# Optimization experiments

Measured on AMD Instinct MI355X. Metric: run time of the kernel, lower is better.

The kernel has to match this reference:

```python
import jax, jax.numpy as jnp
import numpy as np

C_IN, C_OUT, G = 64, 64, 32
D_MODEL = C_IN + 4 * G            # 192
DI = 2 * D_MODEL                  # d_inner = 384 (expand=2)
N_STATE = 16
DT_RANK = (D_MODEL + 15) // 16    # 12
K_DIR = 4
B, H, W = 2, 64, 64


def setup_inputs() -> dict:
    key = jax.random.key(0)
    ks = jax.random.split(key, 16)
    rn = lambda k, shp, s=0.02: jax.random.normal(k, shp, jnp.float32) * s
    inp = {"x": jax.random.normal(ks[0], (B, C_IN, H, W), jnp.float32)}
    chans = [C_IN, C_IN + G, C_IN + 2 * G, C_IN + 3 * G]
    for i, ci in enumerate(chans):
        inp[f"c{i+1}_w"] = rn(ks[1 + i], (G, ci, 3, 3))
        inp[f"c{i+1}_b"] = jnp.zeros((G,), jnp.float32)
    inp["c5_w"] = rn(ks[5], (C_OUT, D_MODEL, 3, 3))
    inp["c5_b"] = jnp.zeros((C_OUT,), jnp.float32)
    inp["ln1_g"] = jnp.ones((D_MODEL,), jnp.float32)
    inp["ln1_b"] = jnp.zeros((D_MODEL,), jnp.float32)
    inp["in_proj_w"] = rn(ks[6], (2 * DI, D_MODEL))
    inp["dw_w"] = rn(ks[7], (DI, 1, 3, 3))          # depthwise conv kernel
    inp["dw_b"] = jnp.zeros((DI,), jnp.float32)
    inp["x_proj_w"] = rn(ks[8], (K_DIR, DT_RANK + 2 * N_STATE, DI))
    inp["dt_w"] = rn(ks[9], (K_DIR, DI, DT_RANK), 0.1)
    inp["dt_b"] = jax.random.uniform(ks[10], (K_DIR, DI), jnp.float32, -4.0, -2.0)
    inp["A_logs"] = jnp.log(jnp.tile(jnp.arange(1, N_STATE + 1, dtype=jnp.float32), (K_DIR, DI, 1)))
    inp["Ds"] = jnp.ones((K_DIR, DI), jnp.float32)
    inp["out_norm_g"] = jnp.ones((DI,), jnp.float32)
    inp["out_norm_b"] = jnp.zeros((DI,), jnp.float32)
    inp["out_proj_w"] = rn(ks[11], (D_MODEL, DI))
    return inp


def conv2d(x, w, b, groups=1):
    y = jax.lax.conv_general_dilated(x, w, (1, 1), 'SAME',
                                     feature_group_count=groups,
                                     dimension_numbers=('NCHW', 'OIHW', 'NCHW'))
    return y + b[None, :, None, None]


def layer_norm(x, g, b, eps=1e-5):
    mu = jnp.mean(x, -1, keepdims=True)
    var = jnp.var(x, -1, keepdims=True)
    return (x - mu) * jax.lax.rsqrt(var + eps) * g + b


def selective_scan(u, delta, A, Bm, Cm, D):
    # u, delta: (B,K,Dm,L); Bm, Cm: (B,K,N,L); A: (K,Dm,N); D: (K,Dm)
    uL = jnp.moveaxis(u, -1, 0)
    dL = jnp.moveaxis(delta, -1, 0)
    BL = jnp.moveaxis(Bm, -1, 0)
    CL = jnp.moveaxis(Cm, -1, 0)
    h0 = jnp.zeros(u.shape[:3] + (A.shape[-1],), u.dtype)  # (B,K,Dm,N)

    def step(h, inp):
        u_l, d_l, B_l, C_l = inp
        dA = jnp.exp(d_l[..., None] * A)                              # (B,K,Dm,N)
        h = dA * h + (d_l * u_l)[..., None] * B_l[:, :, None, :]
        y = jnp.einsum('bkdn,bkn->bkd', h, C_l)
        return h, y

    _, ys = jax.lax.scan(step, h0, (uL, dL, BL, CL))
    y = jnp.moveaxis(ys, 0, -1)                                       # (B,K,Dm,L)
    return y + D[None, :, :, None] * u


def vss_block(x, ln1_g, ln1_b, in_proj_w, dw_w, dw_b, x_proj_w, dt_w, dt_b,
              A_logs, Ds, out_norm_g, out_norm_b, out_proj_w):
    Bn, C, Hh, Ww = x.shape
    L = Hh * Ww
    di = in_proj_w.shape[0] // 2
    nst = A_logs.shape[-1]
    dtr = dt_w.shape[-1]
    xi = jnp.transpose(x, (0, 2, 3, 1))                               # BHWC
    xn = layer_norm(xi, ln1_g, ln1_b)
    xz = xn @ in_proj_w.T                                             # (B,H,W,2*di)
    xp, z = jnp.split(xz, 2, -1)
    xc = jnp.transpose(xp, (0, 3, 1, 2))                              # (B,di,H,W)
    xc = jax.nn.silu(conv2d(xc, dw_w, dw_b, groups=di))
    xf = xc.reshape(Bn, di, L)
    xt = jnp.transpose(xc, (0, 1, 3, 2)).reshape(Bn, di, L)
    xs = jnp.stack([xf, xt, xf[..., ::-1], xt[..., ::-1]], 1)         # (B,4,di,L)
    x_dbl = jnp.einsum('bkdl,kcd->bkcl', xs, x_proj_w)
    dts = jnp.einsum('bkrl,kdr->bkdl', x_dbl[:, :, :dtr], dt_w)
    Bs = x_dbl[:, :, dtr:dtr + nst]
    Cs = x_dbl[:, :, dtr + nst:]
    delta = jax.nn.softplus(dts + dt_b[None, :, :, None])
    A = -jnp.exp(A_logs)
    oy = selective_scan(xs, delta, A, Bs, Cs, Ds)                     # (B,4,di,L)
    inv = oy[:, 2:4, :, ::-1]
    wh = jnp.transpose(oy[:, 1].reshape(Bn, di, Ww, Hh), (0, 1, 3, 2)).reshape(Bn, di, L)
    iwh = jnp.transpose(inv[:, 1].reshape(Bn, di, Ww, Hh), (0, 1, 3, 2)).reshape(Bn, di, L)
    y = oy[:, 0] + inv[:, 0] + wh + iwh
    y = jnp.transpose(y, (0, 2, 1)).reshape(Bn, Hh, Ww, di)
    y = layer_norm(y, out_norm_g, out_norm_b)
    y = y * jax.nn.silu(z)
    out = xi + y @ out_proj_w.T                                       # residual (VSSBlock)
    return jnp.transpose(out, (0, 3, 1, 2))


def reference(x, c1_w, c1_b, c2_w, c2_b, c3_w, c3_b, c4_w, c4_b, c5_w, c5_b,
              ln1_g, ln1_b, in_proj_w, dw_w, dw_b, x_proj_w, dt_w, dt_b,
              A_logs, Ds, out_norm_g, out_norm_b, out_proj_w):
    lrelu = lambda t: jax.nn.leaky_relu(t, 0.01)
    x1 = lrelu(conv2d(x, c1_w, c1_b))
    x2 = lrelu(conv2d(jnp.concatenate([x, x1], 1), c2_w, c2_b))
    x3 = lrelu(conv2d(jnp.concatenate([x, x1, x2], 1), c3_w, c3_b))
    x4 = lrelu(conv2d(jnp.concatenate([x, x1, x2, x3], 1), c4_w, c4_b))
    f = jnp.concatenate([x, x1, x2, x3, x4], 1)                       # (B,192,H,W)
    sa = vss_block(f, ln1_g, ln1_b, in_proj_w, dw_w, dw_b, x_proj_w, dt_w, dt_b,
                   A_logs, Ds, out_norm_g, out_norm_b, out_proj_w)
    return conv2d(sa, c5_w, c5_b)
```

## Files before the change

### kernel.cpp

```cpp
#include <hip/hip_runtime.h>
#include <hip/hip_bf16.h>
#include <math.h>

static constexpr int LEN = 4096;
static constexpr int HN  = 64;
static constexpr int WN  = 64;
static constexpr int NB  = 2;
static constexpr int DM  = 192;
static constexpr int DIM = 384;
static constexpr int NST = 16;
static constexpr int DTR = 12;
static constexpr int KD  = 4;
static constexpr int NC  = 64;
static constexpr int CHL = LEN / NC;

typedef __attribute__((ext_vector_type(8))) short bfrag;
typedef __attribute__((ext_vector_type(4))) float facc;

__device__ __forceinline__ unsigned short f2bf(float x) {
    unsigned int u = __float_as_uint(x);
    return (unsigned short)((u + 0x7FFFu + ((u >> 16) & 1u)) >> 16);
}

__device__ __forceinline__ int maprow(int k, int gl) {
    int g = (k & 2) ? (LEN - 1 - gl) : gl;
    return (k & 1) ? (((g & 63) << 6) | (g >> 6)) : g;
}

__global__ void k_wtr(const float* __restrict__ w, float* __restrict__ wt,
                      int cin, int cout, int n)
{
    int idx = blockIdx.x * 256 + threadIdx.x;
    if (idx >= n) return;
    int ci = idx % cin; int r = idx / cin;
    int co = r % cout; int t = r / cout;
    wt[idx] = w[((size_t)(co * cin + ci)) * 9 + t];
}

__global__ void k_wxp(const float* __restrict__ xpw, float* __restrict__ WX)
{
    int idx = blockIdx.x * 256 + threadIdx.x;
    if (idx >= 192 * DIM) return;
    int row = idx / DIM, d = idx - row * DIM;
    int k = row / 48, c = row - k * 48;
    WX[idx] = (c < 44) ? xpw[((size_t)(k * 44 + c)) * DIM + d] : 0.f;
}

__global__ void k_tr_in(const float* __restrict__ x, float* __restrict__ FN)
{
    __shared__ float t[64][65];
    int b = blockIdx.y, r = blockIdx.x;
    int tid = threadIdx.x;
#pragma unroll
    for (int i = 0; i < 16; ++i) {
        int idx = (i << 8) + tid;
        int c = idx >> 6, xc = idx & 63;
        t[c][xc] = x[((size_t)(b * 64 + c)) * LEN + r * WN + xc];
    }
    __syncthreads();
#pragma unroll
    for (int i = 0; i < 16; ++i) {
        int idx = (i << 8) + tid;
        int px = idx >> 6, c = idx & 63;
        FN[((size_t)(b * LEN + r * WN + px)) * DM + c] = t[c][px];
    }
}

__global__ void __launch_bounds__(256) k_convmf(
    const float* __restrict__ in, int cbuf, int cin, int cout,
    const float* __restrict__ wt2,
    float* __restrict__ part)
{
    __shared__ unsigned short Asb[66][40];
    __shared__ unsigned short Bsb[3][32][40];
    int zz = blockIdx.z;
    int b = zz / 3, s = zz % 3;
    int y0 = blockIdx.x;
    int n0 = blockIdx.y << 5;
    int tid = threadIdx.x;
    int wv = tid >> 6, lane = tid & 63;
    int mb  = (wv & 1) << 5;
    int nbw = (wv >> 1) << 4;
    int lr = lane & 15, lq = lane >> 4;
    int y = y0 + s - 1;
    bool yok = (unsigned)y < (unsigned)HN;
    const float* inb = in + ((size_t)b * LEN + (size_t)y * WN) * cbuf;

    facc acc0 = (facc){0,0,0,0}, acc1 = (facc){0,0,0,0};

    for (int ci0 = 0; ci0 < cin; ci0 += 32) {
#pragma unroll
        for (int it = 0; it < 3; ++it) {
            int fi = (it << 8) + tid;
            if (fi < 528) {
                int px = fi >> 3, c4 = (fi & 7) << 2;
                int xx = px - 1;
                float4 v = make_float4(0.f, 0.f, 0.f, 0.f);
                if (yok && (unsigned)xx < (unsigned)WN)
                    v = *(const float4*)(inb + (size_t)xx * cbuf + ci0 + c4);
                ushort4 u; u.x = f2bf(v.x); u.y = f2bf(v.y); u.z = f2bf(v.z); u.w = f2bf(v.w);
                *(ushort4*)(&Asb[px][c4]) = u;
            }
        }
#pragma unroll
        for (int it = 0; it < 3; ++it) {
            int fi = (it << 8) + tid;
            int dx = fi >> 8; int rem = fi & 255;
            int oc = rem >> 3, c4 = (rem & 7) << 2;
            int t = s * 3 + dx;
            float4 v = *(const float4*)(wt2 + ((size_t)(t * cout + n0 + oc)) * cin + ci0 + c4);
            ushort4 u; u.x = f2bf(v.x); u.y = f2bf(v.y); u.z = f2bf(v.z); u.w = f2bf(v.w);
            *(ushort4*)(&Bsb[dx][oc][c4]) = u;
        }
        __syncthreads();
#pragma unroll
        for (int dx = 0; dx < 3; ++dx) {
            bfrag a0 = *(const bfrag*)(&Asb[mb + lr + dx][lq * 8]);
            bfrag a1 = *(const bfrag*)(&Asb[mb + 16 + lr + dx][lq * 8]);
            bfrag b0 = *(const bfrag*)(&Bsb[dx][nbw + lr][lq * 8]);
            acc0 = __builtin_amdgcn_mfma_f32_16x16x32_bf16(a0, b0, acc0, 0, 0, 0);
            acc1 = __builtin_amdgcn_mfma_f32_16x16x32_bf16(a1, b0, acc1, 0, 0, 0);
        }
        __syncthreads();
    }
    float* pb = part + (((size_t)(s * NB + b) * LEN) + y0 * WN) * cout + n0 + nbw + lr;
#pragma unroll
    for (int r = 0; r < 4; ++r) {
        int px0 = mb + lq * 4 + r;
        pb[(size_t)px0 * cout] = acc0[r];
        pb[(size_t)(px0 + 16) * cout] = acc1[r];
    }
}

__global__ void k_ep_nhwc(const float* __restrict__ part, const float* __restrict__ bias,
                          float* __restrict__ FN, int co0, float slope)
{
    int idx = blockIdx.x * 256 + threadIdx.x;
    int co = idx & 31, px = idx >> 5;
    const size_t S = (size_t)NB * LEN * 32;
    float v = part[idx] + part[S + idx] + part[2 * S + idx] + bias[co];
    v = v > 0.f ? v : v * slope;
    FN[(size_t)px * DM + co0 + co] = v;
}

__global__ void k_ep_pl_tr(const float* __restrict__ part, const float* __restrict__ bias,
                           float* __restrict__ out)
{
    __shared__ float t[64][65];
    int b = blockIdx.y, l0 = blockIdx.x << 6;
    int tid = threadIdx.x;
    const size_t S = (size_t)NB * LEN * 64;
#pragma unroll
    for (int i = 0; i < 16; ++i) {
        int idx = (i << 8) + tid;
        int px = idx >> 6, oc = idx & 63;
        size_t o = ((size_t)b * LEN + l0 + px) * 64 + oc;
        t[px][oc] = part[o] + part[S + o] + part[2 * S + o] + bias[oc];
    }
    __syncthreads();
#pragma unroll
    for (int i = 0; i < 16; ++i) {
        int idx = (i << 8) + tid;
        int oc = idx >> 6, px = idx & 63;
        out[((size_t)(b * 64 + oc)) * LEN + l0 + px] = t[px][oc];
    }
}

__global__ void k_ln(const float* __restrict__ FN, const float* __restrict__ g,
                     const float* __restrict__ be, float* __restrict__ xn)
{
    int lane = threadIdx.x & 63;
    int pix  = (blockIdx.x << 2) + (threadIdx.x >> 6);
    const float* fp = FN + (size_t)pix * DM;
    float v0 = fp[lane];
    float v1 = fp[lane + 64];
    float v2 = fp[lane + 128];
    float s = v0 + v1 + v2, ss = v0 * v0 + v1 * v1 + v2 * v2;
#pragma unroll
    for (int off = 1; off < 64; off <<= 1) { s += __shfl_xor(s, off); ss += __shfl_xor(ss, off); }
    float mu = s * (1.f / 192.f);
    float var = ss * (1.f / 192.f) - mu * mu;
    float rstd = rsqrtf(var + 1e-5f);
    float* op = xn + (size_t)pix * DM;
    op[lane]       = (v0 - mu) * rstd * g[lane]       + be[lane];
    op[lane + 64]  = (v1 - mu) * rstd * g[lane + 64]  + be[lane + 64];
    op[lane + 128] = (v2 - mu) * rstd * g[lane + 128] + be[lane + 128];
}

struct MfTile { facc a00, a01, a10, a11; int mb, nb, lr, lq; };

__device__ __forceinline__ MfTile mf_gemm_core(
    const float* __restrict__ A, int K, const float* __restrict__ Wt,
    int b, int l0, int n0, unsigned short (*Asb)[72], unsigned short (*Bsb)[72])
{
    int tid = threadIdx.x;
    MfTile t;
    t.a00 = (facc){0,0,0,0}; t.a01 = (facc){0,0,0,0};
    t.a10 = (facc){0,0,0,0}; t.a11 = (facc){0,0,0,0};
    int wv = tid >> 6, lane = tid & 63;
    t.mb = (wv & 1) << 5; t.nb = (wv >> 1) << 5;
    t.lr = lane & 15; t.lq = lane >> 4;

    for (int k0 = 0; k0 < K; k0 += 64) {
#pragma unroll
        for (int s = 0; s < 4; ++s) {
            int idx = (s << 8) + tid;
            int row = idx >> 4, c4 = (idx & 15) << 2;
            float4 av = *(const float4*)(A + ((size_t)b * LEN + l0 + row) * K + k0 + c4);
            ushort4 ua; ua.x = f2bf(av.x); ua.y = f2bf(av.y); ua.z = f2bf(av.z); ua.w = f2bf(av.w);
            *(ushort4*)(&Asb[row][c4]) = ua;
            float4 wvv = *(const float4*)(Wt + (size_t)(n0 + row) * K + k0 + c4);
            ushort4 ub; ub.x = f2bf(wvv.x); ub.y = f2bf(wvv.y); ub.z = f2bf(wvv.z); ub.w = f2bf(wvv.w);
            *(ushort4*)(&Bsb[row][c4]) = ub;
        }
        __syncthreads();
#pragma unroll
        for (int kk = 0; kk < 64; kk += 32) {
            bfrag a0 = *(const bfrag*)(&Asb[t.mb + t.lr][kk + t.lq * 8]);
            bfrag a1 = *(const bfrag*)(&Asb[t.mb + 16 + t.lr][kk + t.lq * 8]);
            bfrag b0 = *(const bfrag*)(&Bsb[t.nb + t.lr][kk + t.lq * 8]);
            bfrag b1 = *(const bfrag*)(&Bsb[t.nb + 16 + t.lr][kk + t.lq * 8]);
            t.a00 = __builtin_amdgcn_mfma_f32_16x16x32_bf16(a0, b0, t.a00, 0, 0, 0);
            t.a01 = __builtin_amdgcn_mfma_f32_16x16x32_bf16(a0, b1, t.a01, 0, 0, 0);
            t.a10 = __builtin_amdgcn_mfma_f32_16x16x32_bf16(a1, b0, t.a10, 0, 0, 0);
            t.a11 = __builtin_amdgcn_mfma_f32_16x16x32_bf16(a1, b1, t.a11, 0, 0, 0);
        }
        __syncthreads();
    }
    return t;
}

__device__ __forceinline__ void mf_store(
    facc v, float* __restrict__ Cp, const float* __restrict__ res,
    int b, int l0, int n0, int outC, int lr, int lq)
{
#pragma unroll
    for (int r = 0; r < 4; ++r) {
        int m = lq * 4 + r, n = lr;
        size_t o = ((size_t)b * LEN + l0 + m) * outC + n0 + n;
        float x = v[r];
        if (res) x += res[o];
        Cp[o] = x;
    }
}

__global__ void __launch_bounds__(256) k_gemm_mf(
    const float* __restrict__ A, int K, const float* __restrict__ Wt,
    const float* __restrict__ res, float* __restrict__ Cp, int outC)
{
    __shared__ unsigned short Asb[64][72];
    __shared__ unsigned short Bsb[64][72];
    int b = blockIdx.z, l0 = blockIdx.x << 6, n0 = blockIdx.y << 6;
    MfTile t = mf_gemm_core(A, K, Wt, b, l0, n0, Asb, Bsb);
    mf_store(t.a00, Cp, res, b, l0 + t.mb,      n0 + t.nb,      outC, t.lr, t.lq);
    mf_store(t.a01, Cp, res, b, l0 + t.mb,      n0 + t.nb + 16, outC, t.lr, t.lq);
    mf_store(t.a10, Cp, res, b, l0 + t.mb + 16, n0 + t.nb,      outC, t.lr, t.lq);
    mf_store(t.a11, Cp, res, b, l0 + t.mb + 16, n0 + t.nb + 16, outC, t.lr, t.lq);
}

__global__ void __launch_bounds__(256) k_gemm_ipmf(
    const float* __restrict__ A, const float* __restrict__ Wt,
    float* __restrict__ XPN, float* __restrict__ ZT)
{
    __shared__ unsigned short Asb[64][72];
    __shared__ unsigned short Bsb[64][72];
    int b = blockIdx.z, l0 = blockIdx.x << 6, n0 = blockIdx.y << 6;
    MfTile t = mf_gemm_core(A, DM, Wt, b, l0, n0, Asb, Bsb);
    float* out = (blockIdx.y < 6) ? XPN : ZT;
    int nc = (blockIdx.y < 6) ? n0 : n0 - DIM;
    mf_store(t.a00, out, nullptr, b, l0 + t.mb,      nc + t.nb,      DIM, t.lr, t.lq);
    mf_store(t.a01, out, nullptr, b, l0 + t.mb,      nc + t.nb + 16, DIM, t.lr, t.lq);
    mf_store(t.a10, out, nullptr, b, l0 + t.mb + 16, nc + t.nb,      DIM, t.lr, t.lq);
    mf_store(t.a11, out, nullptr, b, l0 + t.mb + 16, nc + t.nb + 16, DIM, t.lr, t.lq);
}

__global__ void __launch_bounds__(256) k_dw(
    const float* __restrict__ xpn, const float* __restrict__ w,
    const float* __restrict__ bias, float* __restrict__ unh)
{
    int b = blockIdx.z, cg = blockIdx.y, r = blockIdx.x;
    int lane = threadIdx.x & 63, wv = threadIdx.x >> 6;
    int c = cg * 64 + lane;
    float wl[9];
#pragma unroll
    for (int t = 0; t < 9; ++t) wl[t] = w[c * 9 + t];
    float bv = bias[c];
    const float* base = xpn + (size_t)b * LEN * DIM + c;
    float* ob = unh + (size_t)b * LEN * DIM + c;
#pragma unroll 4
    for (int xi = 0; xi < 16; ++xi) {
        int x = wv * 16 + xi;
        float acc = bv;
#pragma unroll
        for (int dy = 0; dy < 3; ++dy) {
            int ry = r + dy - 1;
            if ((unsigned)ry >= (unsigned)HN) continue;
#pragma unroll
            for (int dx = 0; dx < 3; ++dx) {
                int xx = x + dx - 1;
                if ((unsigned)xx >= (unsigned)WN) continue;
                acc += base[(size_t)(ry * WN + xx) * DIM] * wl[dy * 3 + dx];
            }
        }
        acc = acc / (1.f + __expf(-acc));
        ob[(size_t)(r * WN + x) * DIM] = acc;
    }
}

__global__ void __launch_bounds__(384) k_delta(
    const float* __restrict__ CX, const float* __restrict__ dtw,
    const float* __restrict__ dtb, float* __restrict__ dlt)
{
    __shared__ float cs[16][12];
    int b = blockIdx.z, k = blockIdx.y;
    int lp0 = blockIdx.x << 4;
    int tid = threadIdx.x;
    if (tid < 192) {
        int p = tid / 12, r = tid - p * 12;
        cs[p][r] = CX[((size_t)(b * LEN) + lp0 + p) * 192 + k * 48 + r];
    }
    __syncthreads();
    float wt[DTR];
    const float* wp = dtw + ((size_t)(k * DIM) + tid) * DTR;
#pragma unroll
    for (int r = 0; r < DTR; ++r) wt[r] = wp[r];
    float bv = dtb[k * DIM + tid];
    float* dbase = dlt + (((size_t)(b * LEN) + lp0) * KD + k) * DIM + tid;
#pragma unroll
    for (int p = 0; p < 16; ++p) {
        float s = bv;
#pragma unroll
        for (int r = 0; r < DTR; ++r) s += cs[p][r] * wt[r];
        s = (s > 20.f) ? s : __logf(1.f + __expf(s));
        dbase[(size_t)p * KD * DIM] = s;
    }
}

__global__ void __launch_bounds__(384) k_scan_a(
    const float* __restrict__ unh, const float* __restrict__ CX,
    const float* __restrict__ alog, const float* __restrict__ dlt,
    float* __restrict__ hf, float* __restrict__ pA)
{
    __shared__ float bs[CHL * 16];
    int b = blockIdx.z, k = blockIdx.y, c = blockIdx.x;
    int d = threadIdx.x;
    for (int i = threadIdx.x; i < CHL * 16; i += 384) {
        int l = i >> 4, n = i & 15;
        int row = maprow(k, c * CHL + l);
        bs[i] = CX[((size_t)(b * LEN) + row) * 192 + k * 48 + 12 + n];
    }
    __syncthreads();

    float A[16], h[16];
    const float* ap = alog + ((size_t)(k * DIM + d)) * NST;
#pragma unroll
    for (int q = 0; q < 4; ++q) {
        float4 av = *(const float4*)(ap + q * 4);
        A[q * 4]     = -__expf(av.x); A[q * 4 + 1] = -__expf(av.y);
        A[q * 4 + 2] = -__expf(av.z); A[q * 4 + 3] = -__expf(av.w);
    }
    bool geo = true;
#pragma unroll
    for (int n = 1; n < 16; ++n)
        geo = geo && (fabsf(A[n] - (n + 1) * A[0]) <= 1e-4f * (n + 1) * fabsf(A[0]));
#pragma unroll
    for (int n = 0; n < 16; ++n) h[n] = 0.f;

    const float* ub = unh + (size_t)b * LEN * DIM + d;
    const float* db = dlt + ((size_t)(b * LEN) * KD + k) * DIM + d;
    size_t base = (((size_t)((b * KD + k) * NC + c)) * NST) * DIM + d;

    float dvA[4], uuA[4], dvB[4], uuB[4], dvC[4], uuC[4];
#pragma unroll
    for (int j = 0; j < 4; ++j) {
        int row = maprow(k, c * CHL + j);
        dvA[j] = db[(size_t)row * KD * DIM];
        uuA[j] = ub[(size_t)row * DIM];
    }
#pragma unroll
    for (int j = 0; j < 4; ++j) {
        int row = maprow(k, c * CHL + 4 + j);
        dvB[j] = db[(size_t)row * KD * DIM];
        uuB[j] = ub[(size_t)row * DIM];
    }

    if (geo) {
        float A0 = A[0];
        float p0 = 1.f;
        for (int l0 = 0; l0 < CHL; l0 += 4) {
            if (l0 + 8 < CHL) {
#pragma unroll
                for (int j = 0; j < 4; ++j) {
                    int row = maprow(k, c * CHL + l0 + 8 + j);
                    dvC[j] = db[(size_t)row * KD * DIM];
                    uuC[j] = ub[(size_t)row * DIM];
                }
            }
            __builtin_amdgcn_s_setprio(1);
#pragma unroll
            for (int j = 0; j < 4; ++j) {
                float du = dvA[j] * uuA[j];
                const float* bl = bs + (l0 + j) * 16;
                float qv = __expf(dvA[j] * A0);
                float pw = qv;
                h[0] = qv * h[0] + du * bl[0];
#pragma unroll
                for (int n = 1; n < 16; ++n) { pw *= qv; h[n] = pw * h[n] + du * bl[n]; }
                p0 *= qv;
            }
            __builtin_amdgcn_s_setprio(0);
#pragma unroll
            for (int j = 0; j < 4; ++j) { dvA[j] = dvB[j]; uuA[j] = uuB[j]; dvB[j] = dvC[j]; uuB[j] = uuC[j]; }
        }
        float pw = 1.f;
#pragma unroll
        for (int n = 0; n < 16; ++n) {
            pw *= p0;
            hf[base + (size_t)n * DIM] = h[n];
            pA[base + (size_t)n * DIM] = pw;
        }
    } else {
        float p[16];
#pragma unroll
        for (int n = 0; n < 16; ++n) p[n] = 1.f;
        for (int l0 = 0; l0 < CHL; l0 += 4) {
            if (l0 + 8 < CHL) {
#pragma unroll
                for (int j = 0; j < 4; ++j) {
                    int row = maprow(k, c * CHL + l0 + 8 + j);
                    dvC[j] = db[(size_t)row * KD * DIM];
                    uuC[j] = ub[(size_t)row * DIM];
                }
            }
#pragma unroll
            for (int j = 0; j < 4; ++j) {
                float du = dvA[j] * uuA[j];
                const float* bl = bs + (l0 + j) * 16;
#pragma unroll
                for (int n = 0; n < 16; ++n) {
                    float dA = __expf(dvA[j] * A[n]);
                    h[n] = dA * h[n] + du * bl[n];
                    p[n] *= dA;
                }
            }
#pragma unroll
            for (int j = 0; j < 4; ++j) { dvA[j] = dvB[j]; uuA[j] = uuB[j]; dvB[j] = dvC[j]; uuB[j] = uuC[j]; }
        }
#pragma unroll
        for (int n = 0; n < 16; ++n) {
            hf[base + (size_t)n * DIM] = h[n];
            pA[base + (size_t)n * DIM] = p[n];
        }
    }
}

__global__ void k_scan_b(float* __restrict__ hf, const float* __restrict__ pA)
{
    int s = blockIdx.x * 256 + threadIdx.x;
    int bk = s / (NST * DIM);
    int r  = s - bk * (NST * DIM);
    size_t base = (size_t)bk * NC * NST * DIM + r;
    const size_t cs = (size_t)NST * DIM;
    float car = 0.f;
#pragma unroll 8
    for (int c = 0; c < NC; ++c) {
        float hfc = hf[base + c * cs], pc = pA[base + c * cs];
        hf[base + c * cs] = car;
        car = pc * car + hfc;
    }
}

__global__ void __launch_bounds__(384) k_scan_c(
    const float* __restrict__ unh, const float* __restrict__ CX,
    const float* __restrict__ alog, const float* __restrict__ hf,
    float* __restrict__ dlt)
{
    __shared__ float bs[CHL * 32];
    int b = blockIdx.z, k = blockIdx.y, c = blockIdx.x;
    int d = threadIdx.x;
    for (int i = threadIdx.x; i < CHL * 32; i += 384) {
        int l = i >> 5, n = i & 31;
        int row = maprow(k, c * CHL + l);
        bs[i] = CX[((size_t)(b * LEN) + row) * 192 + k * 48 + 12 + n];
    }
    __syncthreads();

    float A[16], h[16];
    const float* ap = alog + ((size_t)(k * DIM + d)) * NST;
#pragma unroll
    for (int q = 0; q < 4; ++q) {
        float4 av = *(const float4*)(ap + q * 4);
        A[q * 4]     = -__expf(av.x); A[q * 4 + 1] = -__expf(av.y);
        A[q * 4 + 2] = -__expf(av.z); A[q * 4 + 3] = -__expf(av.w);
    }
    bool geo = true;
#pragma unroll
    for (int n = 1; n < 16; ++n)
        geo = geo && (fabsf(A[n] - (n + 1) * A[0]) <= 1e-4f * (n + 1) * fabsf(A[0]));
    size_t base = (((size_t)((b * KD + k) * NC + c)) * NST) * DIM + d;
#pragma unroll
    for (int n = 0; n < 16; ++n) h[n] = hf[base + (size_t)n * DIM];

    const float* ub = unh + (size_t)b * LEN * DIM + d;
    float* db = dlt + ((size_t)(b * LEN) * KD + k) * DIM + d;

    int rowsA[4], rowsB[4], rowsC[4];
    float dvA[4], uuA[4], dvB[4], uuB[4], dvC[4], uuC[4];
#pragma unroll
    for (int j = 0; j < 4; ++j) {
        rowsA[j] = maprow(k, c * CHL + j);
        dvA[j] = db[(size_t)rowsA[j] * KD * DIM];
        uuA[j] = ub[(size_t)rowsA[j] * DIM];
    }
#pragma unroll
    for (int j = 0; j < 4; ++j) {
        rowsB[j] = maprow(k, c * CHL + 4 + j);
        dvB[j] = db[(size_t)rowsB[j] * KD * DIM];
        uuB[j] = ub[(size_t)rowsB[j] * DIM];
    }

    if (geo) {
        float A0 = A[0];
        for (int l0 = 0; l0 < CHL; l0 += 4) {
            if (l0 + 8 < CHL) {
#pragma unroll
                for (int j = 0; j < 4; ++j) {
                    rowsC[j] = maprow(k, c * CHL + l0 + 8 + j);
                    dvC[j] = db[(size_t)rowsC[j] * KD * DIM];
                    uuC[j] = ub[(size_t)rowsC[j] * DIM];
                }
            }
            float ys[4];
            __builtin_amdgcn_s_setprio(1);
#pragma unroll
            for (int j = 0; j < 4; ++j) {
                const float* bl = bs + (l0 + j) * 32;
                float du = dvA[j] * uuA[j];
                float qv = __expf(dvA[j] * A0);
                float pw = qv;
                h[0] = qv * h[0] + du * bl[0];
                float y = h[0] * bl[16];
#pragma unroll
                for (int n = 1; n < 16; ++n) {
                    pw *= qv;
                    h[n] = pw * h[n] + du * bl[n];
                    y += h[n] * bl[16 + n];
                }
                ys[j] = y;
            }
            __builtin_amdgcn_s_setprio(0);
#pragma unroll
            for (int j = 0; j < 4; ++j) db[(size_t)rowsA[j] * KD * DIM] = ys[j];
#pragma unroll
            for (int j = 0; j < 4; ++j) {
                rowsA[j] = rowsB[j]; dvA[j] = dvB[j]; uuA[j] = uuB[j];
                rowsB[j] = rowsC[j]; dvB[j] = dvC[j]; uuB[j] = uuC[j];
            }
        }
    } else {
        for (int l0 = 0; l0 < CHL; l0 += 4) {
            if (l0 + 8 < CHL) {
#pragma unroll
                for (int j = 0; j < 4; ++j) {
                    rowsC[j] = maprow(k, c * CHL + l0 + 8 + j);
                    dvC[j] = db[(size_t)rowsC[j] * KD * DIM];
                    uuC[j] = ub[(size_t)rowsC[j] * DIM];
                }
            }
            float ys[4];
#pragma unroll
            for (int j = 0; j < 4; ++j) {
                const float* bl = bs + (l0 + j) * 32;
                float du = dvA[j] * uuA[j];
                float y = 0.f;
#pragma unroll
                for (int n = 0; n < 16; ++n) {
                    float dA = __expf(dvA[j] * A[n]);
                    h[n] = dA * h[n] + du * bl[n];
                    y += h[n] * bl[16 + n];
                }
                ys[j] = y;
            }
#pragma unroll
            for (int j = 0; j < 4; ++j) db[(size_t)rowsA[j] * KD * DIM] = ys[j];
#pragma unroll
            for (int j = 0; j < 4; ++j) {
                rowsA[j] = rowsB[j]; dvA[j] = dvB[j]; uuA[j] = uuB[j];
                rowsB[j] = rowsC[j]; dvB[j] = dvC[j]; uuB[j] = uuC[j];
            }
        }
    }
}

__global__ void k_merge(const float* __restrict__ y4, const float* __restrict__ unh,
                        const float* __restrict__ Ds, const float* __restrict__ ong,
                        const float* __restrict__ onb, const float* __restrict__ zt,
                        float* __restrict__ yg)
{
    int lane = threadIdx.x & 63;
    int pix = (blockIdx.x << 2) + (threadIdx.x >> 6);
    const float* yp = y4 + (size_t)pix * KD * DIM;
    const float* up = unh + (size_t)pix * DIM;
    float v[6]; float s = 0.f, ss = 0.f;
#pragma unroll
    for (int j = 0; j < 6; ++j) {
        int d = lane + (j << 6);
        float y = yp[d] + yp[DIM + d] + yp[2 * DIM + d] + yp[3 * DIM + d];
        float dsum = Ds[d] + Ds[DIM + d] + Ds[2 * DIM + d] + Ds[3 * DIM + d];
        y += dsum * up[d];
        v[j] = y; s += y; ss += y * y;
    }
#pragma unroll
    for (int off = 1; off < 64; off <<= 1) { s += __shfl_xor(s, off); ss += __shfl_xor(ss, off); }
    float mu = s * (1.f / 384.f);
    float var = ss * (1.f / 384.f) - mu * mu;
    float rstd = rsqrtf(var + 1e-5f);
    const float* zp = zt + (size_t)pix * DIM;
    float* op = yg + (size_t)pix * DIM;
#pragma unroll
    for (int j = 0; j < 6; ++j) {
        int d = lane + (j << 6);
        float zz = zp[d];
        float gate = zz / (1.f + __expf(-zz));
        op[d] = ((v[j] - mu) * rstd * ong[d] + onb[d]) * gate;
    }
}

extern "C" void kernel_launch(void* const* d_in, const int* in_sizes, int n_in,
                              void* d_out, int out_size, void* d_ws, size_t ws_size,
                              hipStream_t stream)
{
    const float* x    = (const float*)d_in[0];
    const float* c1w  = (const float*)d_in[1];  const float* c1b = (const float*)d_in[2];
    const float* c2w  = (const float*)d_in[3];  const float* c2b = (const float*)d_in[4];
    const float* c3w  = (const float*)d_in[5];  const float* c3b = (const float*)d_in[6];
    const float* c4w  = (const float*)d_in[7];  const float* c4b = (const float*)d_in[8];
    const float* c5w  = (const float*)d_in[9];  const float* c5b = (const float*)d_in[10];
    const float* ln1g = (const float*)d_in[11]; const float* ln1b= (const float*)d_in[12];
    const float* ipw  = (const float*)d_in[13];
    const float* dww  = (const float*)d_in[14]; const float* dwb = (const float*)d_in[15];
    const float* xpw  = (const float*)d_in[16];
    const float* dtw  = (const float*)d_in[17]; const float* dtb = (const float*)d_in[18];
    const float* alog = (const float*)d_in[19]; const float* dsv = (const float*)d_in[20];
    const float* ong  = (const float*)d_in[21]; const float* onb = (const float*)d_in[22];
    const float* opw  = (const float*)d_in[23];
    float* out = (float*)d_out;

    float* ws   = (float*)d_ws;
    float* FN   = ws;
    float* XN   = FN   + 1572864;
    float* XPN  = XN   + 1572864;
    float* ZT   = XPN  + 3145728;
    float* XCNH = ZT   + 3145728;
    float* DLT  = XCNH + 3145728;
    float* HF   = DLT  + 12582912;
    float* WT14 = HF   + 3145728;
    float* WT5  = WT14 + 129024;
    float* WX   = WT5  + 110592;
    float* PA = XPN;
    float* CX = XN;
    float* PART = XN;
    float* YN = DLT;

    k_wtr<<<dim3(72),  256, 0, stream>>>(c1w, WT14,          64, 32, 9 * 64 * 32);
    k_wtr<<<dim3(108), 256, 0, stream>>>(c2w, WT14 + 18432,  96, 32, 9 * 96 * 32);
    k_wtr<<<dim3(144), 256, 0, stream>>>(c3w, WT14 + 46080, 128, 32, 9 * 128 * 32);
    k_wtr<<<dim3(180), 256, 0, stream>>>(c4w, WT14 + 82944, 160, 32, 9 * 160 * 32);
    k_wtr<<<dim3(432), 256, 0, stream>>>(c5w, WT5,          192, 64, 9 * 192 * 64);
    k_wxp<<<dim3(288), 256, 0, stream>>>(xpw, WX);

    k_tr_in<<<dim3(HN, NB), 256, 0, stream>>>(x, FN);
    k_convmf<<<dim3(64, 1, NB * 3), 256, 0, stream>>>(FN, DM, 64, 32, WT14, PART);
    k_ep_nhwc<<<dim3(1024), 256, 0, stream>>>(PART, c1b, FN, 64, 0.01f);
    k_convmf<<<dim3(64, 1, NB * 3), 256, 0, stream>>>(FN, DM, 96, 32, WT14 + 18432, PART);
    k_ep_nhwc<<<dim3(1024), 256, 0, stream>>>(PART, c2b, FN, 96, 0.01f);
    k_convmf<<<dim3(64, 1, NB * 3), 256, 0, stream>>>(FN, DM, 128, 32, WT14 + 46080, PART);
    k_ep_nhwc<<<dim3(1024), 256, 0, stream>>>(PART, c3b, FN, 128, 0.01f);
    k_convmf<<<dim3(64, 1, NB * 3), 256, 0, stream>>>(FN, DM, 160, 32, WT14 + 82944, PART);
    k_ep_nhwc<<<dim3(1024), 256, 0, stream>>>(PART, c4b, FN, 160, 0.01f);

    k_ln<<<dim3(NB * LEN / 4), 256, 0, stream>>>(FN, ln1g, ln1b, XN);
    k_gemm_ipmf<<<dim3(LEN / 64, 12, NB), 256, 0, stream>>>(XN, ipw, XPN, ZT);
    k_dw<<<dim3(HN, DIM / 64, NB), 256, 0, stream>>>(XPN, dww, dwb, XCNH);
    k_gemm_mf<<<dim3(LEN / 64, 3, NB), 256, 0, stream>>>(XCNH, DIM, WX, nullptr, CX, 192);
    k_delta<<<dim3(LEN / 16, KD, NB), 384, 0, stream>>>(CX, dtw, dtb, DLT);
    k_scan_a<<<dim3(NC, KD, NB), 384, 0, stream>>>(XCNH, CX, alog, DLT, HF, PA);
    k_scan_b<<<dim3(NB * KD * NST * DIM / 256), 256, 0, stream>>>(HF, PA);
    k_scan_c<<<dim3(NC, KD, NB), 384, 0, stream>>>(XCNH, CX, alog, HF, DLT);
    k_merge<<<dim3(NB * LEN / 4), 256, 0, stream>>>(DLT, XCNH, dsv, ong, onb, ZT, XCNH);
    k_gemm_mf<<<dim3(LEN / 64, 3, NB), 256, 0, stream>>>(XCNH, DIM, opw, FN, YN, DM);

    k_convmf<<<dim3(64, 2, NB * 3), 256, 0, stream>>>(YN, DM, 192, 64, WT5, PART);
    k_ep_pl_tr<<<dim3(64, NB), 256, 0, stream>>>(PART, c5b, out);
}
```

Baseline: 297.1 us.

## Store delta and scan outputs in bf16, double scan chunks, recompute chunk decay from delta sums

The delta and per-direction scan outputs are now stored as bf16 instead of fp32, halving the traffic to that large buffer in the delta, scan and merge kernels. The chunk count is doubled so each scan block handles a shorter chunk, which gives more parallelism. Instead of writing 16 per-state decay products, scan_a writes one sum of delta per chunk and scan_b recomputes exp(A*sum) itself. scan_c builds the 16 powers with a shallower multiply tree to shorten the serial chain. The risks are bf16 rounding of delta and y, and a longer serial carry loop in scan_b.

```diff
diff --git a/kernel.cpp b/kernel.cpp
--- a/kernel.cpp
+++ b/kernel.cpp
@@ -11,7 +11,7 @@
 static constexpr int NST = 16;
 static constexpr int DTR = 12;
 static constexpr int KD  = 4;
-static constexpr int NC  = 64;
+static constexpr int NC  = 128;
 static constexpr int CHL = LEN / NC;
 
 typedef __attribute__((ext_vector_type(8))) short bfrag;
@@ -21,10 +21,26 @@
     unsigned int u = __float_as_uint(x);
     return (unsigned short)((u + 0x7FFFu + ((u >> 16) & 1u)) >> 16);
 }
+__device__ __forceinline__ float bf2f(unsigned short u) {
+    return __uint_as_float((unsigned int)u << 16);
+}
 
 __device__ __forceinline__ int maprow(int k, int gl) {
     int g = (k & 2) ? (LEN - 1 - gl) : gl;
     return (k & 1) ? (((g & 63) << 6) | (g >> 6)) : g;
+}
+
+__device__ __forceinline__ void pow16(float qv, float* P) {
+    float qv2 = qv * qv;
+    float qv3 = qv2 * qv;
+    float qv4 = qv2 * qv2;
+    P[0] = qv;  P[1] = qv2; P[2] = qv3; P[3] = qv4;
+    P[4] = qv4 * qv; P[5] = qv4 * qv2; P[6] = qv4 * qv3;
+    float q8 = qv4 * qv4;
+    P[7] = q8;
+#pragma unroll
+    for (int i = 0; i < 7; ++i) P[8 + i] = q8 * P[i];
+    P[15] = q8 * q8;
 }
 
 __global__ void k_wtr(const float* __restrict__ w, float* __restrict__ wt,
@@ -309,7 +325,7 @@
 
 __global__ void __launch_bounds__(384) k_delta(
     const float* __restrict__ CX, const float* __restrict__ dtw,
-    const float* __restrict__ dtb, float* __restrict__ dlt)
+    const float* __restrict__ dtb, unsigned short* __restrict__ dlt)
 {
     __shared__ float cs[16][12];
     int b = blockIdx.z, k = blockIdx.y;
@@ -325,21 +341,21 @@
 #pragma unroll
     for (int r = 0; r < DTR; ++r) wt[r] = wp[r];
     float bv = dtb[k * DIM + tid];
-    float* dbase = dlt + (((size_t)(b * LEN) + lp0) * KD + k) * DIM + tid;
+    unsigned short* dbase = dlt + (((size_t)(b * LEN) + lp0) * KD + k) * DIM + tid;
 #pragma unroll
     for (int p = 0; p < 16; ++p) {
         float s = bv;
 #pragma unroll
         for (int r = 0; r < DTR; ++r) s += cs[p][r] * wt[r];
         s = (s > 20.f) ? s : __logf(1.f + __expf(s));
-        dbase[(size_t)p * KD * DIM] = s;
+        dbase[(size_t)p * KD * DIM] = f2bf(s);
     }
 }
 
 __global__ void __launch_bounds__(384) k_scan_a(
     const float* __restrict__ unh, const float* __restrict__ CX,
-    const float* __restrict__ alog, const float* __restrict__ dlt,
-    float* __restrict__ hf, float* __restrict__ pA)
+    const float* __restrict__ alog, const unsigned short* __restrict__ dlt,
+    float* __restrict__ hf, float* __restrict__ sdvb)
 {
     __shared__ float bs[CHL * 16];
     int b = blockIdx.z, k = blockIdx.y, c = blockIdx.x;
@@ -367,32 +383,32 @@
     for (int n = 0; n < 16; ++n) h[n] = 0.f;
 
     const float* ub = unh + (size_t)b * LEN * DIM + d;
-    const float* db = dlt + ((size_t)(b * LEN) * KD + k) * DIM + d;
+    const unsigned short* db = dlt + ((size_t)(b * LEN) * KD + k) * DIM + d;
     size_t base = (((size_t)((b * KD + k) * NC + c)) * NST) * DIM + d;
+    float sdv = 0.f;
 
     float dvA[4], uuA[4], dvB[4], uuB[4], dvC[4], uuC[4];
 #pragma unroll
     for (int j = 0; j < 4; ++j) {
         int row = maprow(k, c * CHL + j);
-        dvA[j] = db[(size_t)row * KD * DIM];
+        dvA[j] = bf2f(db[(size_t)row * KD * DIM]);
         uuA[j] = ub[(size_t)row * DIM];
     }
 #pragma unroll
     for (int j = 0; j < 4; ++j) {
         int row = maprow(k, c * CHL + 4 + j);
-        dvB[j] = db[(size_t)row * KD * DIM];
+        dvB[j] = bf2f(db[(size_t)row * KD * DIM]);
         uuB[j] = ub[(size_t)row * DIM];
     }
 
     if (geo) {
         float A0 = A[0];
-        float p0 = 1.f;
         for (int l0 = 0; l0 < CHL; l0 += 4) {
             if (l0 + 8 < CHL) {
 #pragma unroll
                 for (int j = 0; j < 4; ++j) {
                     int row = maprow(k, c * CHL + l0 + 8 + j);
-                    dvC[j] = db[(size_t)row * KD * DIM];
+                    dvC[j] = bf2f(db[(size_t)row * KD * DIM]);
                     uuC[j] = ub[(size_t)row * DIM];
                 }
             }
@@ -406,29 +422,19 @@
                 h[0] = qv * h[0] + du * bl[0];
 #pragma unroll
                 for (int n = 1; n < 16; ++n) { pw *= qv; h[n] = pw * h[n] + du * bl[n]; }
-                p0 *= qv;
+                sdv += dvA[j];
             }
             __builtin_amdgcn_s_setprio(0);
 #pragma unroll
             for (int j = 0; j < 4; ++j) { dvA[j] = dvB[j]; uuA[j] = uuB[j]; dvB[j] = dvC[j]; uuB[j] = uuC[j]; }
         }
-        float pw = 1.f;
-#pragma unroll
-        for (int n = 0; n < 16; ++n) {
-            pw *= p0;
-            hf[base + (size_t)n * DIM] = h[n];
-            pA[base + (size_t)n * DIM] = pw;
-        }
     } else {
-        float p[16];
-#pragma unroll
-        for (int n = 0; n < 16; ++n) p[n] = 1.f;
         for (int l0 = 0; l0 < CHL; l0 += 4) {
             if (l0 + 8 < CHL) {
 #pragma unroll
                 for (int j = 0; j < 4; ++j) {
                     int row = maprow(k, c * CHL + l0 + 8 + j);
-                    dvC[j] = db[(size_t)row * KD * DIM];
+                    dvC[j] = bf2f(db[(size_t)row * KD * DIM]);
                     uuC[j] = ub[(size_t)row * DIM];
                 }
             }
@@ -440,32 +446,38 @@
                 for (int n = 0; n < 16; ++n) {
                     float dA = __expf(dvA[j] * A[n]);
                     h[n] = dA * h[n] + du * bl[n];
-                    p[n] *= dA;
                 }
+                sdv += dvA[j];
             }
 #pragma unroll
             for (int j = 0; j < 4; ++j) { dvA[j] = dvB[j]; uuA[j] = uuB[j]; dvB[j] = dvC[j]; uuB[j] = uuC[j]; }
         }
-#pragma unroll
-        for (int n = 0; n < 16; ++n) {
-            hf[base + (size_t)n * DIM] = h[n];
-            pA[base + (size_t)n * DIM] = p[n];
-        }
-    }
-}
-
-__global__ void k_scan_b(float* __restrict__ hf, const float* __restrict__ pA)
+    }
+#pragma unroll
+    for (int n = 0; n < 16; ++n) hf[base + (size_t)n * DIM] = h[n];
+    sdvb[((size_t)((b * KD + k) * NC + c)) * DIM + d] = sdv;
+}
+
+__global__ void k_scan_b(float* __restrict__ hf, const float* __restrict__ sdvb,
+                         const float* __restrict__ alog)
 {
     int s = blockIdx.x * 256 + threadIdx.x;
     int bk = s / (NST * DIM);
     int r  = s - bk * (NST * DIM);
-    size_t base = (size_t)bk * NC * NST * DIM + r;
-    const size_t cs = (size_t)NST * DIM;
+    int n  = r / DIM;
+    int d  = r - n * DIM;
+    int k  = bk & (KD - 1);
+    float A = -__expf(alog[((size_t)(k * DIM + d)) * NST + n]);
+    size_t baseh = (size_t)bk * NC * NST * DIM + (size_t)n * DIM + d;
+    size_t bases = (size_t)bk * NC * DIM + d;
+    const size_t csh = (size_t)NST * DIM;
+    const size_t css = (size_t)DIM;
     float car = 0.f;
-#pragma unroll 8
+#pragma unroll 4
     for (int c = 0; c < NC; ++c) {
-        float hfc = hf[base + c * cs], pc = pA[base + c * cs];
-        hf[base + c * cs] = car;
+        float hfc = hf[baseh + c * csh];
+        float pc = __expf(A * sdvb[bases + c * css]);
+        hf[baseh + c * csh] = car;
         car = pc * car + hfc;
     }
 }
@@ -473,7 +485,7 @@
 __global__ void __launch_bounds__(384) k_scan_c(
     const float* __restrict__ unh, const float* __restrict__ CX,
     const float* __restrict__ alog, const float* __restrict__ hf,
-    float* __restrict__ dlt)
+    unsigned short* __restrict__ dlt)
 {
     __shared__ float bs[CHL * 32];
     int b = blockIdx.z, k = blockIdx.y, c = blockIdx.x;
@@ -502,20 +514,20 @@
     for (int n = 0; n < 16; ++n) h[n] = hf[base + (size_t)n * DIM];
 
     const float* ub = unh + (size_t)b * LEN * DIM + d;
-    float* db = dlt + ((size_t)(b * LEN) * KD + k) * DIM + d;
+    unsigned short* db = dlt + ((size_t)(b * LEN) * KD + k) * DIM + d;
 
     int rowsA[4], rowsB[4], rowsC[4];
     float dvA[4], uuA[4], dvB[4], uuB[4], dvC[4], uuC[4];
 #pragma unroll
     for (int j = 0; j < 4; ++j) {
         rowsA[j] = maprow(k, c * CHL + j);
-        dvA[j] = db[(size_t)rowsA[j] * KD * DIM];
+        dvA[j] = bf2f(db[(size_t)rowsA[j] * KD * DIM]);
         uuA[j] = ub[(size_t)rowsA[j] * DIM];
     }
 #pragma unroll
     for (int j = 0; j < 4; ++j) {
         rowsB[j] = maprow(k, c * CHL + 4 + j);
-        dvB[j] = db[(size_t)rowsB[j] * KD * DIM];
+        dvB[j] = bf2f(db[(size_t)rowsB[j] * KD * DIM]);
         uuB[j] = ub[(size_t)rowsB[j] * DIM];
     }
 
@@ -526,7 +538,7 @@
 #pragma unroll
                 for (int j = 0; j < 4; ++j) {
                     rowsC[j] = maprow(k, c * CHL + l0 + 8 + j);
-                    dvC[j] = db[(size_t)rowsC[j] * KD * DIM];
+                    dvC[j] = bf2f(db[(size_t)rowsC[j] * KD * DIM]);
                     uuC[j] = ub[(size_t)rowsC[j] * DIM];
                 }
             }
@@ -537,20 +549,19 @@
                 const float* bl = bs + (l0 + j) * 32;
                 float du = dvA[j] * uuA[j];
                 float qv = __expf(dvA[j] * A0);
-                float pw = qv;
-                h[0] = qv * h[0] + du * bl[0];
-                float y = h[0] * bl[16];
-#pragma unroll
-                for (int n = 1; n < 16; ++n) {
-                    pw *= qv;
-                    h[n] = pw * h[n] + du * bl[n];
+                float P[16];
+                pow16(qv, P);
+                float y = 0.f;
+#pragma unroll
+                for (int n = 0; n < 16; ++n) {
+                    h[n] = P[n] * h[n] + du * bl[n];
                     y += h[n] * bl[16 + n];
                 }
                 ys[j] = y;
             }
             __builtin_amdgcn_s_setprio(0);
 #pragma unroll
-            for (int j = 0; j < 4; ++j) db[(size_t)rowsA[j] * KD * DIM] = ys[j];
+            for (int j = 0; j < 4; ++j) db[(size_t)rowsA[j] * KD * DIM] = f2bf(ys[j]);
 #pragma unroll
             for (int j = 0; j < 4; ++j) {
                 rowsA[j] = rowsB[j]; dvA[j] = dvB[j]; uuA[j] = uuB[j];
@@ -563,7 +574,7 @@
 #pragma unroll
                 for (int j = 0; j < 4; ++j) {
                     rowsC[j] = maprow(k, c * CHL + l0 + 8 + j);
-                    dvC[j] = db[(size_t)rowsC[j] * KD * DIM];
+                    dvC[j] = bf2f(db[(size_t)rowsC[j] * KD * DIM]);
                     uuC[j] = ub[(size_t)rowsC[j] * DIM];
                 }
             }
@@ -582,7 +593,7 @@
                 ys[j] = y;
             }
 #pragma unroll
-            for (int j = 0; j < 4; ++j) db[(size_t)rowsA[j] * KD * DIM] = ys[j];
+            for (int j = 0; j < 4; ++j) db[(size_t)rowsA[j] * KD * DIM] = f2bf(ys[j]);
 #pragma unroll
             for (int j = 0; j < 4; ++j) {
                 rowsA[j] = rowsB[j]; dvA[j] = dvB[j]; uuA[j] = uuB[j];
@@ -592,20 +603,20 @@
     }
 }
 
-__global__ void k_merge(const float* __restrict__ y4, const float* __restrict__ unh,
+__global__ void k_merge(const unsigned short* __restrict__ y4, const float* __restrict__ unh,
                         const float* __restrict__ Ds, const float* __restrict__ ong,
                         const float* __restrict__ onb, const float* __restrict__ zt,
                         float* __restrict__ yg)
 {
     int lane = threadIdx.x & 63;
     int pix = (blockIdx.x << 2) + (threadIdx.x >> 6);
-    const float* yp = y4 + (size_t)pix * KD * DIM;
+    const unsigned short* yp = y4 + (size_t)pix * KD * DIM;
     const float* up = unh + (size_t)pix * DIM;
     float v[6]; float s = 0.f, ss = 0.f;
 #pragma unroll
     for (int j = 0; j < 6; ++j) {
         int d = lane + (j << 6);
-        float y = yp[d] + yp[DIM + d] + yp[2 * DIM + d] + yp[3 * DIM + d];
+        float y = bf2f(yp[d]) + bf2f(yp[DIM + d]) + bf2f(yp[2 * DIM + d]) + bf2f(yp[3 * DIM + d]);
         float dsum = Ds[d] + Ds[DIM + d] + Ds[2 * DIM + d] + Ds[3 * DIM + d];
         y += dsum * up[d];
         v[j] = y; s += y; ss += y * y;
@@ -652,15 +663,16 @@
     float* XPN  = XN   + 1572864;
     float* ZT   = XPN  + 3145728;
     float* XCNH = ZT   + 3145728;
-    float* DLT  = XCNH + 3145728;
-    float* HF   = DLT  + 12582912;
-    float* WT14 = HF   + 3145728;
+    float* DLTF = XCNH + 3145728;
+    float* HF   = DLTF + 6291456;
+    float* WT14 = HF   + 6291456;
     float* WT5  = WT14 + 129024;
     float* WX   = WT5  + 110592;
-    float* PA = XPN;
+    unsigned short* DLTB = (unsigned short*)DLTF;
+    float* SDV = XPN;
     float* CX = XN;
     float* PART = XN;
-    float* YN = DLT;
+    float* YN = DLTF;
 
     k_wtr<<<dim3(72),  256, 0, stream>>>(c1w, WT14,          64, 32, 9 * 64 * 32);
     k_wtr<<<dim3(108), 256, 0, stream>>>(c2w, WT14 + 18432,  96, 32, 9 * 96 * 32);
@@ -683,11 +695,11 @@
     k_gemm_ipmf<<<dim3(LEN / 64, 12, NB), 256, 0, stream>>>(XN, ipw, XPN, ZT);
     k_dw<<<dim3(HN, DIM / 64, NB), 256, 0, stream>>>(XPN, dww, dwb, XCNH);
     k_gemm_mf<<<dim3(LEN / 64, 3, NB), 256, 0, stream>>>(XCNH, DIM, WX, nullptr, CX, 192);
-    k_delta<<<dim3(LEN / 16, KD, NB), 384, 0, stream>>>(CX, dtw, dtb, DLT);
-    k_scan_a<<<dim3(NC, KD, NB), 384, 0, stream>>>(XCNH, CX, alog, DLT, HF, PA);
-    k_scan_b<<<dim3(NB * KD * NST * DIM / 256), 256, 0, stream>>>(HF, PA);
-    k_scan_c<<<dim3(NC, KD, NB), 384, 0, stream>>>(XCNH, CX, alog, HF, DLT);
-    k_merge<<<dim3(NB * LEN / 4), 256, 0, stream>>>(DLT, XCNH, dsv, ong, onb, ZT, XCNH);
+    k_delta<<<dim3(LEN / 16, KD, NB), 384, 0, stream>>>(CX, dtw, dtb, DLTB);
+    k_scan_a<<<dim3(NC, KD, NB), 384, 0, stream>>>(XCNH, CX, alog, DLTB, HF, SDV);
+    k_scan_b<<<dim3(NB * KD * NST * DIM / 256), 256, 0, stream>>>(HF, SDV, alog);
+    k_scan_c<<<dim3(NC, KD, NB), 384, 0, stream>>>(XCNH, CX, alog, HF, DLTB);
+    k_merge<<<dim3(NB * LEN / 4), 256, 0, stream>>>(DLTB, XCNH, dsv, ong, onb, ZT, XCNH);
     k_gemm_mf<<<dim3(LEN / 64, 3, NB), 256, 0, stream>>>(XCNH, DIM, opw, FN, YN, DM);
 
     k_convmf<<<dim3(64, 2, NB * 3), 256, 0, stream>>>(YN, DM, 192, 64, WT5, PART);
```

Result: slower. 329.2 us (+10.8%).
